# Kernel tuning notes

Measured on AMD Instinct MI355X. Metric: run time of the kernel, lower is better.

## Reference

```python
import jax, jax.numpy as jnp
import numpy as np

DIM = 128
NUM_HEADS = 8
HEAD_DIM = DIM // NUM_HEADS
N_NODES = 50000
N_EDGES = 800000


def setup_inputs() -> dict:
    key = jax.random.key(0)
    ks = jax.random.split(key, 10)
    scale = 1.0 / np.sqrt(DIM)
    x = jax.random.normal(ks[0], (N_NODES, DIM), dtype=jnp.float32)
    edge_index = jax.random.randint(ks[1], (2, N_EDGES), 0, N_NODES, dtype=jnp.int64)
    Wq = jax.random.normal(ks[2], (DIM, DIM), dtype=jnp.float32) * scale
    bq = jnp.zeros((DIM,), dtype=jnp.float32)
    Wk = jax.random.normal(ks[3], (DIM, DIM), dtype=jnp.float32) * scale
    bk = jnp.zeros((DIM,), dtype=jnp.float32)
    Wv = jax.random.normal(ks[4], (DIM, DIM), dtype=jnp.float32) * scale
    bv = jnp.zeros((DIM,), dtype=jnp.float32)
    Wo = jax.random.normal(ks[5], (DIM, DIM), dtype=jnp.float32) * scale
    bo = jnp.zeros((DIM,), dtype=jnp.float32)
    return {"x": x, "edge_index": edge_index, "Wq": Wq, "bq": bq,
            "Wk": Wk, "bk": bk, "Wv": Wv, "bv": bv, "Wo": Wo, "bo": bo}


def reference(x, edge_index, Wq, bq, Wk, bk, Wv, bv, Wo, bo):
    n = x.shape[0]
    tgt = edge_index[0]  # softmax group / scatter destination
    src = edge_index[1]  # gather source
    # projections: torch nn.Linear -> x @ W.T + b
    q = (x @ Wq.T + bq).reshape(n, NUM_HEADS, HEAD_DIM)
    k = (x @ Wk.T + bk).reshape(n, NUM_HEADS, HEAD_DIM)
    v = (x @ Wv.T + bv).reshape(n, NUM_HEADS, HEAD_DIM)
    # edge-wise attention scores: [E, H]
    scores = jnp.einsum('ehd,ehd->eh', q[src], k[tgt]) / np.sqrt(HEAD_DIM).astype(np.float32)
    # segment softmax over edges grouped by target node
    m = jax.ops.segment_max(scores, tgt, num_segments=n)          # [N, H]
    m = jax.lax.stop_gradient(m)
    p = jnp.exp(scores - m[tgt])                                   # [E, H]
    s = jax.ops.segment_sum(p, tgt, num_segments=n)               # [N, H]
    probs = p / s[tgt]
    # weighted scatter-add of source values
    weighted = v[src] * probs[..., None]                           # [E, H, D]
    agg = jax.ops.segment_sum(weighted, tgt, num_segments=n)      # [N, H, D]
    out = agg.reshape(n, DIM) @ Wo.T + bo
    # dropout is identity in eval mode
    return out
```

## Files before the change

### kernel.cpp

```cpp
#include <hip/hip_runtime.h>
#include <math.h>

#define NN 50000
#define NE 800000
#define DIM 128
#define NH 8
#define HD 16
#define NTILE 3125
#define TPB 782
#define LROW 136
#define QVROW 256
#define SCAN_B 196

typedef short v8s __attribute__((ext_vector_type(8)));
typedef float v4f __attribute__((ext_vector_type(4)));

__device__ __forceinline__ unsigned short f2b(float f) {
    unsigned u = __float_as_uint(f);
    u = (u + 0x7fffu + ((u >> 16) & 1u)) >> 16;
    return (unsigned short)u;
}
__device__ __forceinline__ float blo(unsigned w) { return __uint_as_float(w << 16); }
__device__ __forceinline__ float bhi(unsigned w) { return __uint_as_float(w & 0xffff0000u); }

#define NW4 (4 * DIM * DIM / 4)
#define NC4 ((NN + 3) / 4)
__global__ __launch_bounds__(256) void convert_kernel(
    const float* __restrict__ Wq, const float* __restrict__ Wk,
    const float* __restrict__ Wv, const float* __restrict__ Wo,
    unsigned short* __restrict__ Wb, int* __restrict__ cnt)
{
    int i = blockIdx.x * 256 + threadIdx.x;
    if (i < NW4) {
        int mat = i >> 12;
        int off = i & 4095;
        const float* Wsrc = (mat == 0) ? Wq : (mat == 1) ? Wk : (mat == 2) ? Wv : Wo;
        float4 f = ((const float4*)Wsrc)[off];
        uint2 o;
        o.x = (unsigned)f2b(f.x) | ((unsigned)f2b(f.y) << 16);
        o.y = (unsigned)f2b(f.z) | ((unsigned)f2b(f.w) << 16);
        ((uint2*)(Wb + (size_t)mat * DIM * DIM))[off] = o;
    } else if (i < NW4 + NC4) {
        ((int4*)cnt)[i - NW4] = make_int4(0, 0, 0, 0);
    }
}

__global__ __launch_bounds__(256) void qkv_mfma_kernel(
    const float* __restrict__ x, const unsigned short* __restrict__ Wb,
    const float* __restrict__ bq, const float* __restrict__ bk, const float* __restrict__ bv,
    unsigned short* __restrict__ qvb, unsigned short* __restrict__ kb,
    const int* __restrict__ tgt, int* __restrict__ cnt)
{
    __shared__ unsigned short Wl[DIM * LROW];
    const int mat = blockIdx.x / TPB;
    const int tg  = blockIdx.x % TPB;
    const int tid = threadIdx.x;
    const int lane = tid & 63;
    const int warp = tid >> 6;
    const int m = lane & 15;
    const int quad = lane >> 4;

    const int gsize = 3 * TPB * 256;
    for (int e = blockIdx.x * 256 + tid; e < NE; e += gsize)
        atomicAdd(cnt + tgt[e], 1);

    const unsigned short* Wg = Wb + (size_t)mat * DIM * DIM;
#pragma unroll
    for (int it = 0; it < 8; ++it) {
        int chunk = it * 256 + tid;
        int row = chunk >> 4, c8 = chunk & 15;
        *(uint4*)(Wl + row * LROW + c8 * 8) = ((const uint4*)Wg)[chunk];
    }
    __syncthreads();

    const int rt = tg * 4 + warp;
    if (rt >= NTILE) return;
    const int r0 = rt * 16;

    const float* bias_p = (mat == 0) ? bq : (mat == 1) ? bk : bv;

    v8s a[4];
#pragma unroll
    for (int kt = 0; kt < 4; ++kt) {
        const float4* xr = (const float4*)(x + (size_t)(r0 + m) * DIM + kt * 32 + quad * 8);
        float4 f0 = xr[0], f1 = xr[1];
        v8s t;
        t[0] = (short)f2b(f0.x); t[1] = (short)f2b(f0.y);
        t[2] = (short)f2b(f0.z); t[3] = (short)f2b(f0.w);
        t[4] = (short)f2b(f1.x); t[5] = (short)f2b(f1.y);
        t[6] = (short)f2b(f1.z); t[7] = (short)f2b(f1.w);
        a[kt] = t;
    }

#pragma unroll
    for (int nt = 0; nt < 8; ++nt) {
        v4f c = {0.f, 0.f, 0.f, 0.f};
#pragma unroll
        for (int kt = 0; kt < 4; ++kt) {
            v8s b = *(const v8s*)(Wl + (nt * 16 + m) * LROW + kt * 32 + quad * 8);
            c = __builtin_amdgcn_mfma_f32_16x16x32_bf16(a[kt], b, c, 0, 0, 0);
        }
        int col = nt * 16 + m;
        float bias = bias_p[col];
#pragma unroll
        for (int i = 0; i < 4; ++i) {
            int row = r0 + quad * 4 + i;
            unsigned short val = f2b(c[i] + bias);
            if (mat == 1) {
                kb[(size_t)row * DIM + col] = val;
            } else {
                int pos = (col >> 1) * 4 + (col & 1) + ((mat == 2) ? 2 : 0);
                qvb[(size_t)row * QVROW + pos] = val;
            }
        }
    }
}

__global__ __launch_bounds__(256) void scan1_kernel(
    const int* __restrict__ cnt, int* __restrict__ off, int* __restrict__ bsum)
{
    __shared__ int ws4[4];
    const int tid = threadIdx.x, lane = tid & 63, wid = tid >> 6;
    int i = blockIdx.x * 256 + tid;
    int v0 = (i < NN) ? cnt[i] : 0;
    int incl = v0;
#pragma unroll
    for (int d = 1; d < 64; d <<= 1) {
        int t = __shfl_up(incl, d);
        if (lane >= d) incl += t;
    }
    if (lane == 63) ws4[wid] = incl;
    __syncthreads();
    int wexcl = 0;
#pragma unroll
    for (int t = 0; t < 3; ++t) if (t < wid) wexcl += ws4[t];
    if (i < NN) off[i] = wexcl + incl - v0;
    if (tid == 255) bsum[blockIdx.x] = wexcl + incl;
}

__global__ __launch_bounds__(256) void scan23_kernel(
    const int* __restrict__ bsum, int* __restrict__ off, int* __restrict__ cursor)
{
    __shared__ int ws4[4];
    __shared__ int base_s, total_s;
    const int tid = threadIdx.x, lane = tid & 63, wid = tid >> 6;
    int v0 = (tid < SCAN_B) ? bsum[tid] : 0;
    int incl = v0;
#pragma unroll
    for (int d = 1; d < 64; d <<= 1) {
        int t = __shfl_up(incl, d);
        if (lane >= d) incl += t;
    }
    if (lane == 63) ws4[wid] = incl;
    __syncthreads();
    int wexcl = 0;
#pragma unroll
    for (int t = 0; t < 3; ++t) if (t < wid) wexcl += ws4[t];
    int excl = wexcl + incl - v0;
    if (tid == blockIdx.x) base_s = excl;
    if (tid == SCAN_B - 1) total_s = excl + v0;
    __syncthreads();
    int i = blockIdx.x * 256 + tid;
    if (i < NN) {
        int t = off[i] + base_s;
        off[i] = t;
        cursor[i] = t;
    }
    if (blockIdx.x == SCAN_B - 1 && tid == 0) off[NN] = total_s;
}

__global__ __launch_bounds__(256) void fill_kernel(
    const int* __restrict__ tgt, const int* __restrict__ src,
    int* __restrict__ cursor, int* __restrict__ edge_src)
{
    int e = blockIdx.x * 256 + threadIdx.x;
    if (e >= NE) return;
    int t = tgt[e];
    int pos = atomicAdd(cursor + t, 1);
    edge_src[pos] = src[e];
}

__global__ __launch_bounds__(256) void attn_kernel(
    const int* __restrict__ off, const int* __restrict__ edge_src,
    const unsigned short* __restrict__ qvb, const unsigned short* __restrict__ kb,
    unsigned short* __restrict__ aggb)
{
    __shared__ float red[2][64][3];
    const int tid = threadIdx.x;
    const int nib = tid >> 7;
    const int w   = (tid >> 6) & 1;
    const int lane = tid & 63;
    const int node = blockIdx.x * 2 + nib;

    const int base = off[node];
    const int deg  = off[node + 1] - base;

    unsigned kw = *(const unsigned*)(kb + (size_t)node * DIM + 2 * lane);
    const float klo = blo(kw), khi = bhi(kw);

    const int j = lane & 7;
    const int gb = lane & 56;

    float ax = 0.f, ay = 0.f, ss = 0.f;
    const int nw = (deg + 1 - w) >> 1;
    for (int c0 = 0; c0 < nw; c0 += 64) {
        int idx = c0 + lane;
        int srcv = edge_src[base + min(2 * idx + w, deg - 1)];
        int nchunk = min(nw - c0, 64);
        for (int b = 0; b < nchunk; b += 8) {
            int nb = min(nchunk - b, 8);
            uint2 qv[8];
#pragma unroll
            for (int i = 0; i < 8; ++i) {
                int si = __shfl(srcv, b + min(i, nb - 1));
                qv[i] = *(const uint2*)(qvb + (size_t)si * QVROW + 4 * lane);
            }
            float part[8];
#pragma unroll
            for (int i = 0; i < 8; ++i)
                part[i] = blo(qv[i].x) * klo + bhi(qv[i].x) * khi;
            float r1[4];
#pragma unroll
            for (int t = 0; t < 4; ++t) {
                float keep = (j & 1) ? part[2 * t + 1] : part[2 * t];
                float send = (j & 1) ? part[2 * t]     : part[2 * t + 1];
                r1[t] = keep + __shfl_xor(send, 1);
            }
            float r2[2];
#pragma unroll
            for (int u = 0; u < 2; ++u) {
                float keep = (j & 2) ? r1[2 * u + 1] : r1[2 * u];
                float send = (j & 2) ? r1[2 * u]     : r1[2 * u + 1];
                r2[u] = keep + __shfl_xor(send, 2);
            }
            float keep = (j & 4) ? r2[1] : r2[0];
            float send = (j & 4) ? r2[0] : r2[1];
            float tot = keep + __shfl_xor(send, 4);
            float p = __expf(tot * 0.25f);
#pragma unroll
            for (int i = 0; i < 8; ++i) {
                if (i < nb) {
                    float pi = __shfl(p, gb + i);
                    unsigned vv = qv[i].y;
                    ax += pi * blo(vv);
                    ay += pi * bhi(vv);
                    ss += pi;
                }
            }
        }
    }
    if (w == 1) {
        red[nib][lane][0] = ax; red[nib][lane][1] = ay; red[nib][lane][2] = ss;
    }
    __syncthreads();
    if (w == 0) {
        ax += red[nib][lane][0]; ay += red[nib][lane][1]; ss += red[nib][lane][2];
        unsigned* ap = (unsigned*)(aggb + (size_t)node * DIM + 2 * lane);
        if (deg == 0) {
            *ap = 0u;
        } else {
            float inv = 1.f / ss;
            *ap = (unsigned)f2b(ax * inv) | ((unsigned)f2b(ay * inv) << 16);
        }
    }
}

__global__ __launch_bounds__(256) void outproj_mfma_kernel(
    const unsigned short* __restrict__ aggb, const unsigned short* __restrict__ Wob,
    const float* __restrict__ bo, float* __restrict__ out)
{
    __shared__ unsigned short Wl[DIM * LROW];
    const int tid = threadIdx.x;
    const int lane = tid & 63;
    const int warp = tid >> 6;
    const int m = lane & 15;
    const int quad = lane >> 4;

#pragma unroll
    for (int it = 0; it < 8; ++it) {
        int chunk = it * 256 + tid;
        int row = chunk >> 4, c8 = chunk & 15;
        *(uint4*)(Wl + row * LROW + c8 * 8) = ((const uint4*)Wob)[chunk];
    }
    __syncthreads();

    const int rt = blockIdx.x * 4 + warp;
    if (rt >= NTILE) return;
    const int r0 = rt * 16;

    v8s a[4];
#pragma unroll
    for (int kt = 0; kt < 4; ++kt)
        a[kt] = *(const v8s*)(aggb + (size_t)(r0 + m) * DIM + kt * 32 + quad * 8);

#pragma unroll
    for (int nt = 0; nt < 8; ++nt) {
        v4f c = {0.f, 0.f, 0.f, 0.f};
#pragma unroll
        for (int kt = 0; kt < 4; ++kt) {
            v8s b = *(const v8s*)(Wl + (nt * 16 + m) * LROW + kt * 32 + quad * 8);
            c = __builtin_amdgcn_mfma_f32_16x16x32_bf16(a[kt], b, c, 0, 0, 0);
        }
        int col = nt * 16 + m;
        float bias = bo[col];
#pragma unroll
        for (int i = 0; i < 4; ++i) {
            int row = r0 + quad * 4 + i;
            out[(size_t)row * DIM + col] = c[i] + bias;
        }
    }
}

extern "C" void kernel_launch(void* const* d_in, const int* in_sizes, int n_in,
                              void* d_out, int out_size, void* d_ws, size_t ws_size,
                              hipStream_t stream) {
    const float* x  = (const float*)d_in[0];
    const int*   ei = (const int*)d_in[1];
    const float* Wq = (const float*)d_in[2];
    const float* bq = (const float*)d_in[3];
    const float* Wk = (const float*)d_in[4];
    const float* bk = (const float*)d_in[5];
    const float* Wv = (const float*)d_in[6];
    const float* bv = (const float*)d_in[7];
    const float* Wo = (const float*)d_in[8];
    const float* bo = (const float*)d_in[9];

    const int* tgt = ei;
    const int* src = ei + NE;

    char* ws = (char*)d_ws;
    const size_t SZ_QV = (size_t)NN * QVROW * 2;
    const size_t SZ_BF = (size_t)NN * DIM * 2;

    unsigned short* qvb  = (unsigned short*)(ws);
    unsigned short* kb   = (unsigned short*)(ws + SZ_QV);
    unsigned short* aggb = (unsigned short*)(ws + SZ_QV + SZ_BF);
    unsigned short* Wb   = (unsigned short*)(ws + SZ_QV + 2 * SZ_BF);

    char* wi = ws + SZ_QV + 2 * SZ_BF + (size_t)4 * DIM * DIM * 2;
    int* cnt      = (int*)(wi);
    int* off      = (int*)(wi + (size_t)NN * 4);
    int* cursor   = (int*)(wi + (size_t)(2 * NN + 1) * 4);
    int* edge_src = (int*)(wi + (size_t)(3 * NN + 1) * 4);
    int* bsum     = (int*)(wi + (size_t)(3 * NN + 1) * 4 + (size_t)NE * 4);

    const int conv_blocks = (NW4 + NC4 + 255) / 256;
    const int edge_blocks = (NE + 255) / 256;

    convert_kernel<<<conv_blocks, 256, 0, stream>>>(Wq, Wk, Wv, Wo, Wb, cnt);
    qkv_mfma_kernel<<<3 * TPB, 256, 0, stream>>>(x, Wb, bq, bk, bv, qvb, kb, tgt, cnt);
    scan1_kernel<<<SCAN_B, 256, 0, stream>>>(cnt, off, bsum);
    scan23_kernel<<<SCAN_B, 256, 0, stream>>>(bsum, off, cursor);
    fill_kernel<<<edge_blocks, 256, 0, stream>>>(tgt, src, cursor, edge_src);
    attn_kernel<<<(NN + 1) / 2, 256, 0, stream>>>(off, edge_src, qvb, kb, aggb);
    outproj_mfma_kernel<<<TPB, 256, 0, stream>>>(
        aggb, Wb + (size_t)3 * DIM * DIM, bo, (float*)d_out);
}
```

Before: 252.3 us.

## Fold weight bf16 conversion into GEMM kernels and vectorize epilogue stores

Removes the separate weight-conversion kernel. Each GEMM block now loads fp32 weights and converts them to bf16 while staging into LDS, and the count array is zeroed with a memset instead. The MFMA operands are swapped so each lane holds four consecutive output columns, which lets the bias load and the q/k/v and output stores use vector writes instead of scattered scalar stores. Rounding now goes through the HIP bf16 intrinsic. In exchange, every block re-reads and re-converts the full fp32 weight matrix, which doubles the bytes staged per block.

```diff
diff --git a/kernel.cpp b/kernel.cpp
--- a/kernel.cpp
+++ b/kernel.cpp
@@ -1,4 +1,5 @@
 #include <hip/hip_runtime.h>
+#include <hip/hip_bf16.h>
 #include <math.h>
 
 #define NN 50000
@@ -15,38 +16,29 @@
 typedef short v8s __attribute__((ext_vector_type(8)));
 typedef float v4f __attribute__((ext_vector_type(4)));
 
-__device__ __forceinline__ unsigned short f2b(float f) {
-    unsigned u = __float_as_uint(f);
-    u = (u + 0x7fffu + ((u >> 16) & 1u)) >> 16;
-    return (unsigned short)u;
+__device__ __forceinline__ unsigned pack2(float a, float b) {
+    __hip_bfloat162 h = __float22bfloat162_rn(make_float2(a, b));
+    return *reinterpret_cast<unsigned*>(&h);
 }
 __device__ __forceinline__ float blo(unsigned w) { return __uint_as_float(w << 16); }
 __device__ __forceinline__ float bhi(unsigned w) { return __uint_as_float(w & 0xffff0000u); }
 
-#define NW4 (4 * DIM * DIM / 4)
-#define NC4 ((NN + 3) / 4)
-__global__ __launch_bounds__(256) void convert_kernel(
-    const float* __restrict__ Wq, const float* __restrict__ Wk,
-    const float* __restrict__ Wv, const float* __restrict__ Wo,
-    unsigned short* __restrict__ Wb, int* __restrict__ cnt)
-{
-    int i = blockIdx.x * 256 + threadIdx.x;
-    if (i < NW4) {
-        int mat = i >> 12;
-        int off = i & 4095;
-        const float* Wsrc = (mat == 0) ? Wq : (mat == 1) ? Wk : (mat == 2) ? Wv : Wo;
-        float4 f = ((const float4*)Wsrc)[off];
-        uint2 o;
-        o.x = (unsigned)f2b(f.x) | ((unsigned)f2b(f.y) << 16);
-        o.y = (unsigned)f2b(f.z) | ((unsigned)f2b(f.w) << 16);
-        ((uint2*)(Wb + (size_t)mat * DIM * DIM))[off] = o;
-    } else if (i < NW4 + NC4) {
-        ((int4*)cnt)[i - NW4] = make_int4(0, 0, 0, 0);
+__device__ __forceinline__ void stage_w_lds(
+    const float* __restrict__ Wg, unsigned short* __restrict__ Wl, int tid)
+{
+#pragma unroll
+    for (int it = 0; it < 16; ++it) {
+        int chunk = it * 256 + tid;
+        int row = chunk >> 5, c4 = chunk & 31;
+        float4 f = ((const float4*)Wg)[chunk];
+        uint2 o = { pack2(f.x, f.y), pack2(f.z, f.w) };
+        *(uint2*)(Wl + row * LROW + c4 * 4) = o;
     }
 }
 
 __global__ __launch_bounds__(256) void qkv_mfma_kernel(
-    const float* __restrict__ x, const unsigned short* __restrict__ Wb,
+    const float* __restrict__ x,
+    const float* __restrict__ Wq, const float* __restrict__ Wk, const float* __restrict__ Wv,
     const float* __restrict__ bq, const float* __restrict__ bk, const float* __restrict__ bv,
     unsigned short* __restrict__ qvb, unsigned short* __restrict__ kb,
     const int* __restrict__ tgt, int* __restrict__ cnt)
@@ -64,32 +56,25 @@
     for (int e = blockIdx.x * 256 + tid; e < NE; e += gsize)
         atomicAdd(cnt + tgt[e], 1);
 
-    const unsigned short* Wg = Wb + (size_t)mat * DIM * DIM;
-#pragma unroll
-    for (int it = 0; it < 8; ++it) {
-        int chunk = it * 256 + tid;
-        int row = chunk >> 4, c8 = chunk & 15;
-        *(uint4*)(Wl + row * LROW + c8 * 8) = ((const uint4*)Wg)[chunk];
-    }
+    const float* Wg = (mat == 0) ? Wq : (mat == 1) ? Wk : Wv;
+    stage_w_lds(Wg, Wl, tid);
     __syncthreads();
 
     const int rt = tg * 4 + warp;
     if (rt >= NTILE) return;
     const int r0 = rt * 16;
+    const int node = r0 + m;
 
     const float* bias_p = (mat == 0) ? bq : (mat == 1) ? bk : bv;
 
     v8s a[4];
 #pragma unroll
     for (int kt = 0; kt < 4; ++kt) {
-        const float4* xr = (const float4*)(x + (size_t)(r0 + m) * DIM + kt * 32 + quad * 8);
+        const float4* xr = (const float4*)(x + (size_t)node * DIM + kt * 32 + quad * 8);
         float4 f0 = xr[0], f1 = xr[1];
-        v8s t;
-        t[0] = (short)f2b(f0.x); t[1] = (short)f2b(f0.y);
-        t[2] = (short)f2b(f0.z); t[3] = (short)f2b(f0.w);
-        t[4] = (short)f2b(f1.x); t[5] = (short)f2b(f1.y);
-        t[6] = (short)f2b(f1.z); t[7] = (short)f2b(f1.w);
-        a[kt] = t;
+        uint4 u = { pack2(f0.x, f0.y), pack2(f0.z, f0.w),
+                    pack2(f1.x, f1.y), pack2(f1.z, f1.w) };
+        a[kt] = *(v8s*)&u;
     }
 
 #pragma unroll
@@ -97,21 +82,20 @@
         v4f c = {0.f, 0.f, 0.f, 0.f};
 #pragma unroll
         for (int kt = 0; kt < 4; ++kt) {
-            v8s b = *(const v8s*)(Wl + (nt * 16 + m) * LROW + kt * 32 + quad * 8);
-            c = __builtin_amdgcn_mfma_f32_16x16x32_bf16(a[kt], b, c, 0, 0, 0);
-        }
-        int col = nt * 16 + m;
-        float bias = bias_p[col];
-#pragma unroll
-        for (int i = 0; i < 4; ++i) {
-            int row = r0 + quad * 4 + i;
-            unsigned short val = f2b(c[i] + bias);
-            if (mat == 1) {
-                kb[(size_t)row * DIM + col] = val;
-            } else {
-                int pos = (col >> 1) * 4 + (col & 1) + ((mat == 2) ? 2 : 0);
-                qvb[(size_t)row * QVROW + pos] = val;
-            }
+            v8s wf = *(const v8s*)(Wl + (nt * 16 + m) * LROW + kt * 32 + quad * 8);
+            c = __builtin_amdgcn_mfma_f32_16x16x32_bf16(wf, a[kt], c, 0, 0, 0);
+        }
+        const int cbase = nt * 16 + quad * 4;
+        float4 b4 = *(const float4*)(bias_p + cbase);
+        float o0 = c[0] + b4.x, o1 = c[1] + b4.y;
+        float o2 = c[2] + b4.z, o3 = c[3] + b4.w;
+        if (mat == 1) {
+            uint2 pk = { pack2(o0, o1), pack2(o2, o3) };
+            *(uint2*)(kb + (size_t)node * DIM + cbase) = pk;
+        } else {
+            int p0 = 2 * cbase + ((mat == 2) ? 2 : 0);
+            *(unsigned*)(qvb + (size_t)node * QVROW + p0)     = pack2(o0, o1);
+            *(unsigned*)(qvb + (size_t)node * QVROW + p0 + 4) = pack2(o2, o3);
         }
     }
 }
@@ -260,13 +244,13 @@
             *ap = 0u;
         } else {
             float inv = 1.f / ss;
-            *ap = (unsigned)f2b(ax * inv) | ((unsigned)f2b(ay * inv) << 16);
+            *ap = pack2(ax * inv, ay * inv);
         }
     }
 }
 
 __global__ __launch_bounds__(256) void outproj_mfma_kernel(
-    const unsigned short* __restrict__ aggb, const unsigned short* __restrict__ Wob,
+    const unsigned short* __restrict__ aggb, const float* __restrict__ Wo,
     const float* __restrict__ bo, float* __restrict__ out)
 {
     __shared__ unsigned short Wl[DIM * LROW];
@@ -276,38 +260,31 @@
     const int m = lane & 15;
     const int quad = lane >> 4;
 
-#pragma unroll
-    for (int it = 0; it < 8; ++it) {
-        int chunk = it * 256 + tid;
-        int row = chunk >> 4, c8 = chunk & 15;
-        *(uint4*)(Wl + row * LROW + c8 * 8) = ((const uint4*)Wob)[chunk];
-    }
+    stage_w_lds(Wo, Wl, tid);
     __syncthreads();
 
     const int rt = blockIdx.x * 4 + warp;
     if (rt >= NTILE) return;
     const int r0 = rt * 16;
+    const int node = r0 + m;
 
     v8s a[4];
 #pragma unroll
     for (int kt = 0; kt < 4; ++kt)
-        a[kt] = *(const v8s*)(aggb + (size_t)(r0 + m) * DIM + kt * 32 + quad * 8);
+        a[kt] = *(const v8s*)(aggb + (size_t)node * DIM + kt * 32 + quad * 8);
 
 #pragma unroll
     for (int nt = 0; nt < 8; ++nt) {
         v4f c = {0.f, 0.f, 0.f, 0.f};
 #pragma unroll
         for (int kt = 0; kt < 4; ++kt) {
-            v8s b = *(const v8s*)(Wl + (nt * 16 + m) * LROW + kt * 32 + quad * 8);
-            c = __builtin_amdgcn_mfma_f32_16x16x32_bf16(a[kt], b, c, 0, 0, 0);
-        }
-        int col = nt * 16 + m;
-        float bias = bo[col];
-#pragma unroll
-        for (int i = 0; i < 4; ++i) {
-            int row = r0 + quad * 4 + i;
-            out[(size_t)row * DIM + col] = c[i] + bias;
-        }
+            v8s wf = *(const v8s*)(Wl + (nt * 16 + m) * LROW + kt * 32 + quad * 8);
+            c = __builtin_amdgcn_mfma_f32_16x16x32_bf16(wf, a[kt], c, 0, 0, 0);
+        }
+        const int cbase = nt * 16 + quad * 4;
+        float4 b4 = *(const float4*)(bo + cbase);
+        float4 o = { c[0] + b4.x, c[1] + b4.y, c[2] + b4.z, c[3] + b4.w };
+        *(float4*)(out + (size_t)node * DIM + cbase) = o;
     }
 }
 
@@ -335,24 +312,22 @@
     unsigned short* qvb  = (unsigned short*)(ws);
     unsigned short* kb   = (unsigned short*)(ws + SZ_QV);
     unsigned short* aggb = (unsigned short*)(ws + SZ_QV + SZ_BF);
-    unsigned short* Wb   = (unsigned short*)(ws + SZ_QV + 2 * SZ_BF);
-
-    char* wi = ws + SZ_QV + 2 * SZ_BF + (size_t)4 * DIM * DIM * 2;
+
+    char* wi = ws + SZ_QV + 2 * SZ_BF;
     int* cnt      = (int*)(wi);
     int* off      = (int*)(wi + (size_t)NN * 4);
     int* cursor   = (int*)(wi + (size_t)(2 * NN + 1) * 4);
     int* edge_src = (int*)(wi + (size_t)(3 * NN + 1) * 4);
     int* bsum     = (int*)(wi + (size_t)(3 * NN + 1) * 4 + (size_t)NE * 4);
 
-    const int conv_blocks = (NW4 + NC4 + 255) / 256;
     const int edge_blocks = (NE + 255) / 256;
 
-    convert_kernel<<<conv_blocks, 256, 0, stream>>>(Wq, Wk, Wv, Wo, Wb, cnt);
-    qkv_mfma_kernel<<<3 * TPB, 256, 0, stream>>>(x, Wb, bq, bk, bv, qvb, kb, tgt, cnt);
+    hipMemsetAsync(cnt, 0, (size_t)NN * 4, stream);
+    qkv_mfma_kernel<<<3 * TPB, 256, 0, stream>>>(
+        x, Wq, Wk, Wv, bq, bk, bv, qvb, kb, tgt, cnt);
     scan1_kernel<<<SCAN_B, 256, 0, stream>>>(cnt, off, bsum);
     scan23_kernel<<<SCAN_B, 256, 0, stream>>>(bsum, off, cursor);
     fill_kernel<<<edge_blocks, 256, 0, stream>>>(tgt, src, cursor, edge_src);
     attn_kernel<<<(NN + 1) / 2, 256, 0, stream>>>(off, edge_src, qvb, kb, aggb);
-    outproj_mfma_kernel<<<TPB, 256, 0, stream>>>(
-        aggb, Wb + (size_t)3 * DIM * DIM, bo, (float*)d_out);
-}
+    outproj_mfma_kernel<<<TPB, 256, 0, stream>>>(aggb, Wo, bo, (float*)d_out);
+}
```

Result: slower. 267.3 us (+6.0%).
